# Optimization experiments

Hardware: AMD Instinct MI355X
Metric: run time of the kernel (lower is better)

## Reference

```python
import jax, jax.numpy as jnp
import numpy as np

T = 1048576  # time-series length
INTERVAL_EPOCH = 10


def setup_inputs() -> dict:
    key = jax.random.key(0)
    x = jax.random.uniform(key, (T, 9), dtype=jnp.float32)
    p = lambda v: jnp.array([v], dtype=jnp.float32)
    return {
        "x": x,
        "f_0": p(0.9), "f_c": p(0.5), "k": p(0.2), "n": p(0.9),
        "d_p": p(0.0001), "evap": p(0.29), "evap_constant": p(0.02),
        "missing_restrict": p(2.0), "missing": p(0.2),
        "w_r_1": p(1.0), "w_r_2": p(1.0), "w_z_1": p(1.0), "w_z_2": p(1.0),
        "epoch": 20,
    }


def _runflow(x, f_0, f_c, k, n, d_p, evap, evap_constant,
             missing_restrict, missing, w_r_1, w_r_2, w_z_1, w_z_2, epoch):
    greenland  = x[:, 0]
    impervious = x[:, 2]
    area       = x[:, 3]
    slope      = x[:, 4]
    prec       = x[:, 6]
    total_prec = x[:, 7]
    area_id    = x[0, 8]

    f0, fc, k0, n0 = f_0[0], f_c[0], k[0], n[0]
    dp, ev, evc = d_p[0], evap[0], evap_constant[0]
    mr, miss = missing_restrict[0], missing[0]
    wr1, wr2, wz1, wz2 = w_r_1[0], w_r_2[0], w_z_1[0], w_z_2[0]

    # --- antecedent precipitation recurrence: prec_pre[i] depends on prec_pre[i-1], prec[i-1]
    pp0 = total_prec[0] - prec[0]

    def pp_step(carry, p_prev):
        last = jnp.where(carry > mr, mr + (carry - mr) * miss, carry)
        new = (last + p_prev) * (1.0 - ev) - evc
        return new, new

    _, pp_tail = jax.lax.scan(pp_step, pp0, prec[:-1])
    prec_pre = jax.nn.relu(jnp.concatenate([pp0[None], pp_tail]))  # [T]

    # --- Horton infiltration + rational/Manning runoff (elementwise)
    f_t = (f0 - fc) * jnp.exp(-(k0 * total_prec)) + fc
    q_greenland = jax.nn.relu(prec_pre / 1000.0 * (greenland * area) * (1.0 - f_t))
    d_imperv = jax.nn.relu(prec_pre / 1000.0 - dp)
    q_imperv = jax.nn.relu(jnp.sqrt(impervious * area) * (1.49 / n0)
                           * d_imperv ** (5.0 / 3.0) * jnp.sqrt(slope))
    q = q_imperv + q_greenland  # [T]

    # --- delay: special catchments (3723, 870) shift by 1 step, others by 4
    rid = jnp.round(area_id)
    shift = jnp.where((rid == 3723.0) | (rid == 870.0), 1, 4)
    idx = jnp.arange(T)
    q_shift = jnp.where(idx < shift, 0.0, q[(idx - shift) % T])  # zero-padded delay

    if epoch > INTERVAL_EPOCH:
        # --- linear RNN routing: h_i = h_{i-1}*wr1 + q_i*wr2 ; q2_i = h_i*wz1 + q_i*wz2
        def rt_step(h, qi):
            h_new = h * wr1 + qi * wr2
            return h_new, h_new * wz1 + qi * wz2

        _, q2_tail = jax.lax.scan(rt_step, jnp.float32(0.0), q_shift[1:])
        q2 = jnp.concatenate([q_shift[:1], q2_tail])
        return q2.reshape(T, 1, 1)
    return q_shift.reshape(T, 1, 1)


def reference(x, f_0, f_c, k, n, d_p, evap, evap_constant,
              missing_restrict, missing, w_r_1, w_r_2, w_z_1, w_z_2, epoch):
    return _runflow(x, f_0, f_c, k, n, d_p, evap, evap_constant,
                    missing_restrict, missing, w_r_1, w_r_2, w_z_1, w_z_2, epoch)
```

## Files before the change

### kernel.cpp

```cpp
#include <hip/hip_runtime.h>

#define T_N     1048576
#define BLK     256
#define S_OUT   8
#define R_BLOCK (BLK * S_OUT)
#define NB      (T_N / R_BLOCK)
#define NTH     (T_N / S_OUT)
#define WARM    64
#define HALO    (WARM + 4)
#define SW(u)   ((u) + ((u) >> 3))

__device__ __forceinline__ float pp_step(float c, float p, float mr, float miss,
                                         float omev, float evc) {
    float last = (c > mr) ? fmaf(c - mr, miss, mr) : c;
    return fmaf(last + p, omev, -evc);
}

__global__ __launch_bounds__(BLK) void k_main(
    const float* __restrict__ x,
    const float* __restrict__ f0p, const float* __restrict__ fcp,
    const float* __restrict__ kp,  const float* __restrict__ nnp,
    const float* __restrict__ dpp, const float* __restrict__ evp,
    const float* __restrict__ evcp,const float* __restrict__ mrp,
    const float* __restrict__ missp,
    const float* __restrict__ wr1p,const float* __restrict__ wr2p,
    const float* __restrict__ wz1p,const float* __restrict__ wz2p,
    const int*   __restrict__ epp,
    float* __restrict__ out, float* __restrict__ Bthr, float* __restrict__ Bblk)
{
    __shared__ float s_prec[SW(R_BLOCK + HALO - 1) + 1];
    __shared__ float s_cG[SW(R_BLOCK + 3) + 1];
    __shared__ float s_cA[SW(R_BLOCK + 3) + 1];
    __shared__ float s_B[BLK];

    const int b = blockIdx.x, t = threadIdx.x;
    const int row0 = b * R_BLOCK;

    const float f0 = *f0p, fc = *fcp, kk = *kp, nn = *nnp;
    const float dp = *dpp, ev = *evp, evc = *evcp, mr = *mrp, miss = *missp;
    const float wr1 = *wr1p, wr2 = *wr2p, wz1 = *wz1p, wz2 = *wz2p;
    const int ep = *epp;
    const float omev = 1.0f - ev;
    const float cimp = 1.49f / nn;
    const float f0mfc = f0 - fc;

    const float rid = rintf(x[8]);
    const int shift = (rid == 3723.0f || rid == 870.0f) ? 1 : 4;
    const float pp0 = x[7] - x[6];

    for (int u = t; u < R_BLOCK + HALO; u += BLK) {
        int r = row0 - HALO + u;
        s_prec[SW(u)] = (r >= 0) ? x[r * 9 + 6] : 0.0f;
    }
    for (int u = t; u < R_BLOCK + 4; u += BLK) {
        int r = row0 - 4 + u;
        float cg = 0.0f, ca = 0.0f;
        if (r >= 0) {
            const float* row = x + r * 9;
            float gl = row[0], imp = row[2], ar = row[3], sl = row[4], tp = row[7];
            float ft = fmaf(f0mfc, __expf(-kk * tp), fc);
            cg = gl * ar * (1.0f - ft) * 0.001f;
            ca = sqrtf(imp * ar) * cimp * sqrtf(sl);
        }
        s_cG[SW(u)] = cg;
        s_cA[SW(u)] = ca;
    }
    __syncthreads();

    const int i0 = row0 + t * S_OUT;
    const int rb = i0 - shift;
    int rr = rb - WARM; if (rr < 0) rr = 0;
    float c = (rr == 0) ? pp0 : 0.0f;
    const int rs = (rb < 0) ? 0 : rb;
    for (; rr < rs; ++rr)
        c = pp_step(c, s_prec[SW(rr - row0 + HALO)], mr, miss, omev, evc);

    float outl[S_OUT];
    float h = 0.0f;
    for (int j = 0; j < S_OUT; ++j) {
        const int i = i0 + j;
        const int r = i - shift;
        float qs = 0.0f;
        if (r >= 0) {
            float pre = fmaxf(c, 0.0f);
            int ci = r - row0 + 4;
            float qg = fmaxf(pre * s_cG[SW(ci)], 0.0f);
            float di = fmaxf(fmaf(pre, 0.001f, -dp), 0.0f);
            float qi = fmaxf(s_cA[SW(ci)] * __powf(di, 5.0f / 3.0f), 0.0f);
            qs = qg + qi;
            c = pp_step(c, s_prec[SW(r - row0 + HALO)], mr, miss, omev, evc);
        }
        h = fmaf(wr1, h, wr2 * qs);
        outl[j] = (ep > 10) ? fmaf(wz1, h, wz2 * qs) : qs;
    }

    float4* op = reinterpret_cast<float4*>(out + i0);
    op[0] = make_float4(outl[0], outl[1], outl[2], outl[3]);
    op[1] = make_float4(outl[4], outl[5], outl[6], outl[7]);

    float Bv = (ep > 10) ? h : 0.0f;
    s_B[t] = Bv;
    Bthr[b * BLK + t] = Bv;
    __syncthreads();
    if (t == 0) {
        const float at = powf(wr1, (float)S_OUT);
        float acc = 0.0f;
        for (int u = 0; u < BLK; ++u) acc = fmaf(at, acc, s_B[u]);
        Bblk[b] = acc;
    }
}

__global__ __launch_bounds__(BLK) void k_fix(
    float* __restrict__ out,
    const float* __restrict__ Bthr, const float* __restrict__ Bblk,
    const float* __restrict__ wr1p, const float* __restrict__ wz1p)
{
    __shared__ float sBb[NB];
    __shared__ float sB[BLK];
    __shared__ float carr[BLK];
    __shared__ float sred[BLK];
    const int b = blockIdx.x, t = threadIdx.x;
    const float wr1 = *wr1p, wz1 = *wz1p;
    for (int u = t; u < NB; u += BLK) sBb[u] = Bblk[u];
    sB[t] = Bthr[b * BLK + t];
    __syncthreads();

    const float ab = powf(wr1, (float)R_BLOCK);
    const float at = powf(wr1, (float)S_OUT);
    float partial = 0.0f;
    for (int u = t; u < b; u += BLK)
        partial = fmaf(sBb[u], powf(ab, (float)(b - 1 - u)), partial);
    sred[t] = partial;
    __syncthreads();
    for (int off = BLK / 2; off > 0; off >>= 1) {
        if (t < off) sred[t] += sred[t + off];
        __syncthreads();
    }
    if (t == 0) {
        float cth = sred[0];
        for (int u = 0; u < BLK; ++u) { carr[u] = cth; cth = fmaf(at, cth, sB[u]); }
    }
    __syncthreads();

    float hin = carr[t];
    if (hin != 0.0f) {
        float4* op = reinterpret_cast<float4*>(out + b * R_BLOCK + t * S_OUT);
        float4 v0 = op[0], v1 = op[1];
        float p = hin * wz1;
        p *= wr1; v0.x += p; p *= wr1; v0.y += p; p *= wr1; v0.z += p; p *= wr1; v0.w += p;
        p *= wr1; v1.x += p; p *= wr1; v1.y += p; p *= wr1; v1.z += p; p *= wr1; v1.w += p;
        op[0] = v0;
        op[1] = v1;
    }
}

extern "C" void kernel_launch(void* const* d_in, const int* in_sizes, int n_in,
                              void* d_out, int out_size, void* d_ws, size_t ws_size,
                              hipStream_t stream) {
    const float* x = (const float*)d_in[0];
    float* out  = (float*)d_out;
    float* Bthr = (float*)d_ws;
    float* Bblk = Bthr + NTH;

    k_main<<<NB, BLK, 0, stream>>>(x,
        (const float*)d_in[1],  (const float*)d_in[2],  (const float*)d_in[3],
        (const float*)d_in[4],  (const float*)d_in[5],  (const float*)d_in[6],
        (const float*)d_in[7],  (const float*)d_in[8],  (const float*)d_in[9],
        (const float*)d_in[10], (const float*)d_in[11], (const float*)d_in[12],
        (const float*)d_in[13], (const int*)d_in[14],
        out, Bthr, Bblk);

    k_fix<<<NB, BLK, 0, stream>>>(out, Bthr, Bblk,
        (const float*)d_in[10], (const float*)d_in[12]);
}
```

Measured before the change: 125.3 us.

## Fuse main and fix kernels into one cooperative kernel with grid sync

Merges the two-pass linear-recurrence routing into a single cooperative launch. Each block publishes its block-level carry, then waits on a grid-wide barrier and applies the carry correction in registers before writing output. This removes the second launch, the per-thread carry round trip through global memory, and the read-modify-write of the output. In exchange it needs all 512 blocks co-resident, which launch bounds of 2 per CU allow on 256 CUs, and it pays for a grid barrier.

```diff
diff --git a/kernel.cpp b/kernel.cpp
--- a/kernel.cpp
+++ b/kernel.cpp
@@ -1,11 +1,13 @@
 #include <hip/hip_runtime.h>
+#include <hip/hip_cooperative_groups.h>
+
+namespace cg = cooperative_groups;
 
 #define T_N     1048576
 #define BLK     256
 #define S_OUT   8
 #define R_BLOCK (BLK * S_OUT)
 #define NB      (T_N / R_BLOCK)
-#define NTH     (T_N / S_OUT)
 #define WARM    64
 #define HALO    (WARM + 4)
 #define SW(u)   ((u) + ((u) >> 3))
@@ -16,7 +18,7 @@
     return fmaf(last + p, omev, -evc);
 }
 
-__global__ __launch_bounds__(BLK) void k_main(
+__global__ __launch_bounds__(BLK, 2) void k_fused(
     const float* __restrict__ x,
     const float* __restrict__ f0p, const float* __restrict__ fcp,
     const float* __restrict__ kp,  const float* __restrict__ nnp,
@@ -26,12 +28,15 @@
     const float* __restrict__ wr1p,const float* __restrict__ wr2p,
     const float* __restrict__ wz1p,const float* __restrict__ wz2p,
     const int*   __restrict__ epp,
-    float* __restrict__ out, float* __restrict__ Bthr, float* __restrict__ Bblk)
+    float* __restrict__ out, float* __restrict__ Bblk)
 {
     __shared__ float s_prec[SW(R_BLOCK + HALO - 1) + 1];
     __shared__ float s_cG[SW(R_BLOCK + 3) + 1];
     __shared__ float s_cA[SW(R_BLOCK + 3) + 1];
     __shared__ float s_B[BLK];
+    __shared__ float sBb[NB];
+    __shared__ float sred[BLK];
+    __shared__ float carr[BLK];
 
     const int b = blockIdx.x, t = threadIdx.x;
     const int row0 = b * R_BLOCK;
@@ -54,15 +59,15 @@
     }
     for (int u = t; u < R_BLOCK + 4; u += BLK) {
         int r = row0 - 4 + u;
-        float cg = 0.0f, ca = 0.0f;
+        float cg_ = 0.0f, ca = 0.0f;
         if (r >= 0) {
             const float* row = x + r * 9;
             float gl = row[0], imp = row[2], ar = row[3], sl = row[4], tp = row[7];
             float ft = fmaf(f0mfc, __expf(-kk * tp), fc);
-            cg = gl * ar * (1.0f - ft) * 0.001f;
+            cg_ = gl * ar * (1.0f - ft) * 0.001f;
             ca = sqrtf(imp * ar) * cimp * sqrtf(sl);
         }
-        s_cG[SW(u)] = cg;
+        s_cG[SW(u)] = cg_;
         s_cA[SW(u)] = ca;
     }
     __syncthreads();
@@ -77,6 +82,7 @@
 
     float outl[S_OUT];
     float h = 0.0f;
+    #pragma unroll
     for (int j = 0; j < S_OUT; ++j) {
         const int i = i0 + j;
         const int r = i - shift;
@@ -94,82 +100,74 @@
         outl[j] = (ep > 10) ? fmaf(wz1, h, wz2 * qs) : qs;
     }
 
+    float Bv = (ep > 10) ? h : 0.0f;
+    s_B[t] = Bv;
+    __syncthreads();
+    const float at = powf(wr1, (float)S_OUT);
+    if (t == 0) {
+        float acc = 0.0f;
+        for (int u = 0; u < BLK; ++u) acc = fmaf(at, acc, s_B[u]);
+        __hip_atomic_store(&Bblk[b], acc, __ATOMIC_RELAXED, __HIP_MEMORY_SCOPE_AGENT);
+    }
+    __threadfence();
+    cg::this_grid().sync();
+
+    float hin = 0.0f;
+    if (ep > 10) {
+        for (int u = t; u < NB; u += BLK)
+            sBb[u] = __hip_atomic_load(&Bblk[u], __ATOMIC_RELAXED, __HIP_MEMORY_SCOPE_AGENT);
+        __syncthreads();
+        const float ab = powf(wr1, (float)R_BLOCK);
+        float partial = 0.0f;
+        for (int u = t; u < b; u += BLK)
+            partial = fmaf(sBb[u], powf(ab, (float)(b - 1 - u)), partial);
+        sred[t] = partial;
+        __syncthreads();
+        for (int off = BLK / 2; off > 0; off >>= 1) {
+            if (t < off) sred[t] += sred[t + off];
+            __syncthreads();
+        }
+        if (t == 0) {
+            float cth = sred[0];
+            for (int u = 0; u < BLK; ++u) { carr[u] = cth; cth = fmaf(at, cth, s_B[u]); }
+        }
+        __syncthreads();
+        hin = carr[t];
+    }
+    if (hin != 0.0f) {
+        float p = hin * wz1;
+        #pragma unroll
+        for (int j = 0; j < S_OUT; ++j) { p *= wr1; outl[j] += p; }
+    }
+
     float4* op = reinterpret_cast<float4*>(out + i0);
     op[0] = make_float4(outl[0], outl[1], outl[2], outl[3]);
     op[1] = make_float4(outl[4], outl[5], outl[6], outl[7]);
-
-    float Bv = (ep > 10) ? h : 0.0f;
-    s_B[t] = Bv;
-    Bthr[b * BLK + t] = Bv;
-    __syncthreads();
-    if (t == 0) {
-        const float at = powf(wr1, (float)S_OUT);
-        float acc = 0.0f;
-        for (int u = 0; u < BLK; ++u) acc = fmaf(at, acc, s_B[u]);
-        Bblk[b] = acc;
-    }
-}
-
-__global__ __launch_bounds__(BLK) void k_fix(
-    float* __restrict__ out,
-    const float* __restrict__ Bthr, const float* __restrict__ Bblk,
-    const float* __restrict__ wr1p, const float* __restrict__ wz1p)
-{
-    __shared__ float sBb[NB];
-    __shared__ float sB[BLK];
-    __shared__ float carr[BLK];
-    __shared__ float sred[BLK];
-    const int b = blockIdx.x, t = threadIdx.x;
-    const float wr1 = *wr1p, wz1 = *wz1p;
-    for (int u = t; u < NB; u += BLK) sBb[u] = Bblk[u];
-    sB[t] = Bthr[b * BLK + t];
-    __syncthreads();
-
-    const float ab = powf(wr1, (float)R_BLOCK);
-    const float at = powf(wr1, (float)S_OUT);
-    float partial = 0.0f;
-    for (int u = t; u < b; u += BLK)
-        partial = fmaf(sBb[u], powf(ab, (float)(b - 1 - u)), partial);
-    sred[t] = partial;
-    __syncthreads();
-    for (int off = BLK / 2; off > 0; off >>= 1) {
-        if (t < off) sred[t] += sred[t + off];
-        __syncthreads();
-    }
-    if (t == 0) {
-        float cth = sred[0];
-        for (int u = 0; u < BLK; ++u) { carr[u] = cth; cth = fmaf(at, cth, sB[u]); }
-    }
-    __syncthreads();
-
-    float hin = carr[t];
-    if (hin != 0.0f) {
-        float4* op = reinterpret_cast<float4*>(out + b * R_BLOCK + t * S_OUT);
-        float4 v0 = op[0], v1 = op[1];
-        float p = hin * wz1;
-        p *= wr1; v0.x += p; p *= wr1; v0.y += p; p *= wr1; v0.z += p; p *= wr1; v0.w += p;
-        p *= wr1; v1.x += p; p *= wr1; v1.y += p; p *= wr1; v1.z += p; p *= wr1; v1.w += p;
-        op[0] = v0;
-        op[1] = v1;
-    }
 }
 
 extern "C" void kernel_launch(void* const* d_in, const int* in_sizes, int n_in,
                               void* d_out, int out_size, void* d_ws, size_t ws_size,
                               hipStream_t stream) {
-    const float* x = (const float*)d_in[0];
+    const float* x    = (const float*)d_in[0];
+    const float* f0p  = (const float*)d_in[1];
+    const float* fcp  = (const float*)d_in[2];
+    const float* kp   = (const float*)d_in[3];
+    const float* nnp  = (const float*)d_in[4];
+    const float* dpp  = (const float*)d_in[5];
+    const float* evp  = (const float*)d_in[6];
+    const float* evcp = (const float*)d_in[7];
+    const float* mrp  = (const float*)d_in[8];
+    const float* missp= (const float*)d_in[9];
+    const float* wr1p = (const float*)d_in[10];
+    const float* wr2p = (const float*)d_in[11];
+    const float* wz1p = (const float*)d_in[12];
+    const float* wz2p = (const float*)d_in[13];
+    const int*   epp  = (const int*)d_in[14];
     float* out  = (float*)d_out;
-    float* Bthr = (float*)d_ws;
-    float* Bblk = Bthr + NTH;
+    float* Bblk = (float*)d_ws;
 
-    k_main<<<NB, BLK, 0, stream>>>(x,
-        (const float*)d_in[1],  (const float*)d_in[2],  (const float*)d_in[3],
-        (const float*)d_in[4],  (const float*)d_in[5],  (const float*)d_in[6],
-        (const float*)d_in[7],  (const float*)d_in[8],  (const float*)d_in[9],
-        (const float*)d_in[10], (const float*)d_in[11], (const float*)d_in[12],
-        (const float*)d_in[13], (const int*)d_in[14],
-        out, Bthr, Bblk);
-
-    k_fix<<<NB, BLK, 0, stream>>>(out, Bthr, Bblk,
-        (const float*)d_in[10], (const float*)d_in[12]);
+    void* args[] = { &x, &f0p, &fcp, &kp, &nnp, &dpp, &evp, &evcp, &mrp, &missp,
+                     &wr1p, &wr2p, &wz1p, &wz2p, &epp, &out, &Bblk };
+    hipLaunchCooperativeKernel((const void*)k_fused, dim3(NB), dim3(BLK),
+                               args, 0, stream);
 }
```

After: 232.4 us. 1.86x slower.

## Halve per-thread outputs and batch global loads into registers before shared stores

Applied to the files above, without the earlier changes.

Halves the outputs per thread from 8 to 4, which doubles the block count and shrinks shared tiles. The staging loops are fully unrolled so all global loads of precipitation and coefficient columns are issued into registers before any compute or shared-memory store, raising memory-level parallelism. Launch bounds now request 4 blocks per CU. The cost is that the 64-step warm-up recurrence is amortized over fewer outputs, so redundant serial work per output roughly doubles, and the k_fix carry chains and thread-level sums get longer.

```diff
diff --git a/kernel.cpp b/kernel.cpp
--- a/kernel.cpp
+++ b/kernel.cpp
@@ -2,13 +2,15 @@
 
 #define T_N     1048576
 #define BLK     256
-#define S_OUT   8
+#define S_OUT   4
 #define R_BLOCK (BLK * S_OUT)
 #define NB      (T_N / R_BLOCK)
 #define NTH     (T_N / S_OUT)
 #define WARM    64
 #define HALO    (WARM + 4)
-#define SW(u)   ((u) + ((u) >> 3))
+#define SW(u)   ((u) + ((u) >> 2))
+#define NPREC   ((R_BLOCK + HALO + BLK - 1) / BLK)
+#define NCOEF   ((R_BLOCK + 4 + BLK - 1) / BLK)
 
 __device__ __forceinline__ float pp_step(float c, float p, float mr, float miss,
                                          float omev, float evc) {
@@ -16,7 +18,7 @@
     return fmaf(last + p, omev, -evc);
 }
 
-__global__ __launch_bounds__(BLK) void k_main(
+__global__ __launch_bounds__(BLK, 4) void k_main(
     const float* __restrict__ x,
     const float* __restrict__ f0p, const float* __restrict__ fcp,
     const float* __restrict__ kp,  const float* __restrict__ nnp,
@@ -48,22 +50,45 @@
     const int shift = (rid == 3723.0f || rid == 870.0f) ? 1 : 4;
     const float pp0 = x[7] - x[6];
 
-    for (int u = t; u < R_BLOCK + HALO; u += BLK) {
+    float pv[NPREC];
+    #pragma unroll
+    for (int i = 0; i < NPREC; ++i) {
+        int u = t + i * BLK;
         int r = row0 - HALO + u;
-        s_prec[SW(u)] = (r >= 0) ? x[r * 9 + 6] : 0.0f;
+        int rc = r < 0 ? 0 : r;
+        if (u >= R_BLOCK + HALO) rc = 0;
+        float ld = x[rc * 9 + 6];
+        pv[i] = (u < R_BLOCK + HALO && r >= 0) ? ld : 0.0f;
     }
-    for (int u = t; u < R_BLOCK + 4; u += BLK) {
+    float v0[NCOEF], v2[NCOEF], v3[NCOEF], v4[NCOEF], v7[NCOEF];
+    #pragma unroll
+    for (int i = 0; i < NCOEF; ++i) {
+        int u = t + i * BLK;
         int r = row0 - 4 + u;
-        float cg = 0.0f, ca = 0.0f;
-        if (r >= 0) {
-            const float* row = x + r * 9;
-            float gl = row[0], imp = row[2], ar = row[3], sl = row[4], tp = row[7];
-            float ft = fmaf(f0mfc, __expf(-kk * tp), fc);
-            cg = gl * ar * (1.0f - ft) * 0.001f;
-            ca = sqrtf(imp * ar) * cimp * sqrtf(sl);
+        bool ok = (u < R_BLOCK + 4) && (r >= 0);
+        int rc = ok ? r : 0;
+        const float* row = x + rc * 9;
+        float l0 = row[0], l2 = row[2], l3 = row[3], l4 = row[4], l7 = row[7];
+        v0[i] = ok ? l0 : 0.0f;
+        v2[i] = ok ? l2 : 0.0f;
+        v3[i] = ok ? l3 : 0.0f;
+        v4[i] = ok ? l4 : 0.0f;
+        v7[i] = ok ? l7 : 0.0f;
+    }
+
+    #pragma unroll
+    for (int i = 0; i < NPREC; ++i) {
+        int u = t + i * BLK;
+        if (u < R_BLOCK + HALO) s_prec[SW(u)] = pv[i];
+    }
+    #pragma unroll
+    for (int i = 0; i < NCOEF; ++i) {
+        int u = t + i * BLK;
+        if (u < R_BLOCK + 4) {
+            float ft = fmaf(f0mfc, __expf(-kk * v7[i]), fc);
+            s_cG[SW(u)] = v0[i] * v3[i] * (1.0f - ft) * 0.001f;
+            s_cA[SW(u)] = sqrtf(v2[i] * v3[i]) * cimp * sqrtf(v4[i]);
         }
-        s_cG[SW(u)] = cg;
-        s_cA[SW(u)] = ca;
     }
     __syncthreads();
 
@@ -77,6 +102,7 @@
 
     float outl[S_OUT];
     float h = 0.0f;
+    #pragma unroll
     for (int j = 0; j < S_OUT; ++j) {
         const int i = i0 + j;
         const int r = i - shift;
@@ -96,7 +122,6 @@
 
     float4* op = reinterpret_cast<float4*>(out + i0);
     op[0] = make_float4(outl[0], outl[1], outl[2], outl[3]);
-    op[1] = make_float4(outl[4], outl[5], outl[6], outl[7]);
 
     float Bv = (ep > 10) ? h : 0.0f;
     s_B[t] = Bv;
@@ -145,12 +170,10 @@
     float hin = carr[t];
     if (hin != 0.0f) {
         float4* op = reinterpret_cast<float4*>(out + b * R_BLOCK + t * S_OUT);
-        float4 v0 = op[0], v1 = op[1];
+        float4 v = op[0];
         float p = hin * wz1;
-        p *= wr1; v0.x += p; p *= wr1; v0.y += p; p *= wr1; v0.z += p; p *= wr1; v0.w += p;
-        p *= wr1; v1.x += p; p *= wr1; v1.y += p; p *= wr1; v1.z += p; p *= wr1; v1.w += p;
-        op[0] = v0;
-        op[1] = v1;
+        p *= wr1; v.x += p; p *= wr1; v.y += p; p *= wr1; v.z += p; p *= wr1; v.w += p;
+        op[0] = v;
     }
 }
 
```

After: 123.1 us. Within noise of the previous version (-1.7%).
